# Kernel tuning notes

Hardware: AMD Instinct MI355X
Metric: run time of the kernel (lower is better)

Reference implementation:

```python
import jax, jax.numpy as jnp
import numpy as np

NUM_HEADS = 12
HEAD_DIM = 64
MASKED_BIAS = -10000.0


def setup_inputs() -> dict:
    key = jax.random.key(0)
    k1, k2, k3 = jax.random.split(key, 3)
    B, S, D = 2, 2048, 768
    return {
        "hidden_states": jax.random.normal(k1, (B, S, D), dtype=jnp.float32),
        "c_attn_w": jax.random.normal(k2, (D, 3 * D), dtype=jnp.float32) * 0.02,
        "c_attn_b": jnp.zeros((3 * D,), dtype=jnp.float32),
        "c_proj_w": jax.random.normal(k3, (D, D), dtype=jnp.float32) * 0.02,
        "c_proj_b": jnp.zeros((D,), dtype=jnp.float32),
    }


def _split_heads(x, B, S):
    # [B,S,D] -> [B,H,S,hd]
    return x.reshape(B, S, NUM_HEADS, HEAD_DIM).transpose(0, 2, 1, 3)


def reference(hidden_states, c_attn_w, c_attn_b, c_proj_w, c_proj_b):
    B, S, D = hidden_states.shape
    qkv = hidden_states @ c_attn_w + c_attn_b  # [B,S,3D]
    q, k, v = jnp.split(qkv, 3, axis=-1)
    q = _split_heads(q, B, S)
    k = _split_heads(k, B, S)
    v = _split_heads(v, B, S)

    # Unfused attention: full [B,H,S,S] scores, where-based causal mask
    attn_weights = jnp.einsum("bhqd,bhkd->bhqk", q, k)
    attn_weights = attn_weights / jnp.float32(HEAD_DIM) ** 0.5
    causal_mask = jnp.tril(jnp.ones((S, S), dtype=bool))[None, None]
    attn_weights = jnp.where(causal_mask, attn_weights,
                             jnp.asarray(MASKED_BIAS, attn_weights.dtype))
    attn_weights = jax.nn.softmax(attn_weights, axis=-1)
    attn_output = jnp.einsum("bhqk,bhkd->bhqd", attn_weights, v)

    # merge heads [B,H,S,hd] -> [B,S,D]
    attn_output = attn_output.transpose(0, 2, 1, 3).reshape(B, S, D)
    attn_output = attn_output @ c_proj_w + c_proj_b
    return attn_output
```

## Files before the change

kernel.cpp:

```cpp
#include <hip/hip_runtime.h>
#include <stdint.h>


constexpr int B_  = 2;
constexpr int S_  = 2048;
constexpr int D_  = 768;
constexpr int N3D = 3 * D_;
constexpr int M_  = B_ * S_;

typedef __bf16 bv8 __attribute__((ext_vector_type(8)));
typedef float  fv4 __attribute__((ext_vector_type(4)));
typedef unsigned short uv4 __attribute__((ext_vector_type(4)));
typedef unsigned short uv8 __attribute__((ext_vector_type(8)));

__device__ inline unsigned short f2bf(float x) {
    union { float f; unsigned int u; } v; v.f = x;
    unsigned int r = v.u + 0x7FFFu + ((v.u >> 16) & 1u);
    return (unsigned short)(r >> 16);
}

__device__ inline fv4 mfma16(bv8 a, bv8 b, fv4 c) {
    return __builtin_amdgcn_mfma_f32_16x16x32_bf16(a, b, c, 0, 0, 0);
}

#define GLOAD_LDS16(g, l)                                                        \
    __builtin_amdgcn_global_load_lds(                                            \
        (__attribute__((address_space(1))) void*)(g),                            \
        (__attribute__((address_space(3))) void*)(l), 16, 0, 0)

#define VMCNT4() asm volatile("s_waitcnt vmcnt(4)" ::: "memory")
#define VMCNT0() asm volatile("s_waitcnt vmcnt(0)" ::: "memory")
#define BAR()                                                                    \
    do { asm volatile("" ::: "memory"); __builtin_amdgcn_s_barrier();            \
         asm volatile("" ::: "memory"); } while (0)

__global__ __launch_bounds__(256)
void cvt_f32_bf16(const float* __restrict__ in, unsigned short* __restrict__ out)
{
    const size_t i = ((size_t)blockIdx.x * 256 + threadIdx.x) * 8;
    const float4 a = *(const float4*)&in[i];
    const float4 b = *(const float4*)&in[i + 4];
    uv8 o;
    o[0] = f2bf(a.x); o[1] = f2bf(a.y); o[2] = f2bf(a.z); o[3] = f2bf(a.w);
    o[4] = f2bf(b.x); o[5] = f2bf(b.y); o[6] = f2bf(b.z); o[7] = f2bf(b.w);
    *(uv8*)&out[i] = o;
}

__global__ __launch_bounds__(256)
void transpose_cvt(const float* __restrict__ W, unsigned short* __restrict__ WT,
                   int K, int N)
{
    __shared__ float tl[32][33];
    const int n0 = blockIdx.x * 32, k0 = blockIdx.y * 32;
    const int t = threadIdx.x;
    {
        const int r = t >> 3, c = (t & 7) * 4;
        const float4 v = *(const float4*)&W[(size_t)(k0 + r) * N + n0 + c];
        tl[r][c + 0] = v.x; tl[r][c + 1] = v.y; tl[r][c + 2] = v.z; tl[r][c + 3] = v.w;
    }
    __syncthreads();
    {
        const int rn = t >> 3, ck = (t & 7) * 4;
        uv4 o;
        o[0] = f2bf(tl[ck + 0][rn]); o[1] = f2bf(tl[ck + 1][rn]);
        o[2] = f2bf(tl[ck + 2][rn]); o[3] = f2bf(tl[ck + 3][rn]);
        *(uv4*)&WT[(size_t)(n0 + rn) * K + k0 + ck] = o;
    }
}

template<bool QKV>
__global__ __launch_bounds__(256)
void gemm_bf16(const unsigned short* __restrict__ A, const unsigned short* __restrict__ BT,
               const float* __restrict__ bias, float* __restrict__ Cf,
               unsigned short* __restrict__ Qb, unsigned short* __restrict__ Kb,
               unsigned short* __restrict__ VTb, int M, int N, int K)
{
    __shared__ unsigned short sA[2][128 * 32];
    __shared__ unsigned short sB[2][128 * 32];
    const int t = threadIdx.x, w = t >> 6, lane = t & 63;
    const int l15 = lane & 15, l4 = lane >> 4;
    const int m0 = blockIdx.y * 128, n0 = blockIdx.x * 128;
    const int wr = w >> 1, wc = w & 1;

    fv4 acc[4][4];
#pragma unroll
    for (int i = 0; i < 4; ++i)
#pragma unroll
        for (int j = 0; j < 4; ++j) acc[i][j] = fv4{0.f, 0.f, 0.f, 0.f};

    const int r0 = w * 16 + (lane >> 2);
    const int c0 = (lane & 3) ^ ((r0 >> 1) & 3);
    const int r1 = (w + 4) * 16 + (lane >> 2);
    const int c1 = (lane & 3) ^ ((r1 >> 1) & 3);

    auto stage = [&](int buf, int k0) {
        GLOAD_LDS16(A  + (size_t)(m0 + r0) * K + k0 + c0 * 8, &sA[buf][w * 512]);
        GLOAD_LDS16(A  + (size_t)(m0 + r1) * K + k0 + c1 * 8, &sA[buf][(w + 4) * 512]);
        GLOAD_LDS16(BT + (size_t)(n0 + r0) * K + k0 + c0 * 8, &sB[buf][w * 512]);
        GLOAD_LDS16(BT + (size_t)(n0 + r1) * K + k0 + c1 * 8, &sB[buf][(w + 4) * 512]);
    };

    stage(0, 0);
    const int nt = K >> 5;
    for (int tt = 0; tt < nt; ++tt) {
        const int cur = tt & 1;
        if (tt + 1 < nt) { stage(cur ^ 1, (tt + 1) * 32); VMCNT4(); }
        else             { VMCNT0(); }
        BAR();

        bv8 af[4], bf[4];
#pragma unroll
        for (int i = 0; i < 4; ++i) {
            const int r = wr * 64 + i * 16 + l15;
            const int c = l4 ^ ((r >> 1) & 3);
            af[i] = *(const bv8*)&sA[cur][r * 32 + c * 8];
        }
#pragma unroll
        for (int j = 0; j < 4; ++j) {
            const int r = wc * 64 + j * 16 + l15;
            const int c = l4 ^ ((r >> 1) & 3);
            bf[j] = *(const bv8*)&sB[cur][r * 32 + c * 8];
        }
#pragma unroll
        for (int i = 0; i < 4; ++i)
#pragma unroll
            for (int j = 0; j < 4; ++j)
                acc[i][j] = mfma16(af[i], bf[j], acc[i][j]);
        BAR();
    }

#pragma unroll
    for (int jf = 0; jf < 4; ++jf) {
        const int col = n0 + wc * 64 + jf * 16 + l15;
        const float bb = bias[col];
        if (QKV) {
            const int sect = col / 768;
            const int rem  = col - sect * 768;
            const int hh_  = rem >> 6, d = rem & 63;
#pragma unroll
            for (int i = 0; i < 4; ++i) {
                const int rowb = m0 + wr * 64 + i * 16 + l4 * 4;
                const size_t bh = (size_t)(rowb >> 11) * 12 + hh_;
                const int s0 = rowb & 2047;
                if (sect == 2) {
                    uv4 pk;
#pragma unroll
                    for (int reg = 0; reg < 4; ++reg) pk[reg] = f2bf(acc[i][jf][reg] + bb);
                    *(uv4*)&VTb[(bh * 64 + d) * 2048 + s0] = pk;
                } else {
                    unsigned short* dst = (sect == 0) ? Qb : Kb;
#pragma unroll
                    for (int reg = 0; reg < 4; ++reg)
                        dst[(bh * 2048 + s0 + reg) * 64 + d] = f2bf(acc[i][jf][reg] + bb);
                }
            }
        } else {
#pragma unroll
            for (int i = 0; i < 4; ++i) {
                const int rowb = m0 + wr * 64 + i * 16 + l4 * 4;
#pragma unroll
                for (int reg = 0; reg < 4; ++reg)
                    Cf[(size_t)(rowb + reg) * N + col] = acc[i][jf][reg] + bb;
            }
        }
    }
}

__global__ __launch_bounds__(256)
void flash_mfma(const unsigned short* __restrict__ Qb, const unsigned short* __restrict__ Kb,
                const unsigned short* __restrict__ VTb, unsigned short* __restrict__ outb)
{
    const int qt = 31 - blockIdx.x;
    const int h  = blockIdx.y, b = blockIdx.z;
    const int bh = b * 12 + h;

    __shared__ unsigned short sK [2][64 * 64];
    __shared__ unsigned short sVT[2][64 * 64];
    __shared__ unsigned short sP [4][16 * 64];

    const int t = threadIdx.x, w = t >> 6, lane = t & 63;
    const int l15 = lane & 15, l4 = lane >> 4;
    const int qrow = qt * 64 + w * 16;

    const int sr0 = w * 8 + (lane >> 3), sc0 = (lane & 7) ^ (sr0 & 7);
    const int sr1 = (w + 4) * 8 + (lane >> 3), sc1 = (lane & 7) ^ (sr1 & 7);
    const unsigned short* Kbase = Kb  + (size_t)bh * 2048 * 64;
    const unsigned short* Vbase = VTb + (size_t)bh * 64 * 2048;

    auto stage = [&](int buf, int kt) {
        GLOAD_LDS16(Kbase + (size_t)(kt * 64 + sr0) * 64 + sc0 * 8, &sK[buf][w * 512]);
        GLOAD_LDS16(Kbase + (size_t)(kt * 64 + sr1) * 64 + sc1 * 8, &sK[buf][(w + 4) * 512]);
        GLOAD_LDS16(Vbase + (size_t)sr0 * 2048 + kt * 64 + sc0 * 8, &sVT[buf][w * 512]);
        GLOAD_LDS16(Vbase + (size_t)sr1 * 2048 + kt * 64 + sc1 * 8, &sVT[buf][(w + 4) * 512]);
    };

    bv8 qf[2];
    {
        const unsigned short* qp = Qb + ((size_t)bh * 2048 + qrow + l15) * 64 + l4 * 8;
        qf[0] = *(const bv8*)qp;
        qf[1] = *(const bv8*)(qp + 32);
    }

    fv4 o[4];
#pragma unroll
    for (int j = 0; j < 4; ++j) o[j] = fv4{0.f, 0.f, 0.f, 0.f};
    float m_ = -1e30f, l_ = 0.f;

    stage(0, 0);
    for (int kt = 0; kt <= qt; ++kt) {
        const int cur = kt & 1;
        if (kt < qt) { stage(cur ^ 1, kt + 1); VMCNT4(); }
        else         { VMCNT0(); }
        BAR();

        fv4 st[4];
#pragma unroll
        for (int jf = 0; jf < 4; ++jf) {
            st[jf] = fv4{0.f, 0.f, 0.f, 0.f};
            const int kr = jf * 16 + l15;
#pragma unroll
            for (int hh = 0; hh < 2; ++hh) {
                const bv8 ka = *(const bv8*)&sK[cur][kr * 64 + (((hh * 4 + l4) ^ (kr & 7)) * 8)];
                st[jf] = mfma16(ka, qf[hh], st[jf]);
            }
        }

        float ps[16];
        const bool dtile = (kt == qt);
        const int qg = qrow + l15;
#pragma unroll
        for (int jf = 0; jf < 4; ++jf)
#pragma unroll
            for (int reg = 0; reg < 4; ++reg) {
                float v = st[jf][reg] * 0.125f;
                if (dtile && (kt * 64 + jf * 16 + l4 * 4 + reg) > qg) v = -10000.0f;
                ps[jf * 4 + reg] = v;
            }

        float rmax = ps[0];
#pragma unroll
        for (int u = 1; u < 16; ++u) rmax = fmaxf(rmax, ps[u]);
        rmax = fmaxf(rmax, __shfl_xor(rmax, 16));
        rmax = fmaxf(rmax, __shfl_xor(rmax, 32));
        const float nm = fmaxf(m_, rmax);
        const float sc = __expf(m_ - nm);
        float psum = 0.f;
#pragma unroll
        for (int u = 0; u < 16; ++u) {
            const float p = __expf(ps[u] - nm);
            ps[u] = p;
            psum += p;
        }
        psum += __shfl_xor(psum, 16);
        psum += __shfl_xor(psum, 32);
        l_ = l_ * sc + psum;
        m_ = nm;

        float scq[4];
#pragma unroll
        for (int reg = 0; reg < 4; ++reg) scq[reg] = __shfl(sc, l4 * 4 + reg);
#pragma unroll
        for (int jf = 0; jf < 4; ++jf)
#pragma unroll
            for (int reg = 0; reg < 4; ++reg) o[jf][reg] *= scq[reg];

#pragma unroll
        for (int jf = 0; jf < 4; ++jf) {
            uv4 pk;
#pragma unroll
            for (int reg = 0; reg < 4; ++reg) pk[reg] = f2bf(ps[jf * 4 + reg]);
            const int chunk = jf * 2 + (l4 >> 1);
            *(uv4*)&sP[w][l15 * 64 + ((chunk ^ (l15 & 7)) * 8) + (l4 & 1) * 4] = pk;
        }

        bv8 pa[2];
#pragma unroll
        for (int hh = 0; hh < 2; ++hh)
            pa[hh] = *(const bv8*)&sP[w][l15 * 64 + (((hh * 4 + l4) ^ (l15 & 7)) * 8)];
#pragma unroll
        for (int jf = 0; jf < 4; ++jf) {
            const int dr = jf * 16 + l15;
#pragma unroll
            for (int hh = 0; hh < 2; ++hh) {
                const bv8 vb = *(const bv8*)&sVT[cur][dr * 64 + (((hh * 4 + l4) ^ (dr & 7)) * 8)];
                o[jf] = mfma16(pa[hh], vb, o[jf]);
            }
        }
        BAR();
    }

    const float inv = 1.0f / l_;
    float invq[4];
#pragma unroll
    for (int reg = 0; reg < 4; ++reg) invq[reg] = __shfl(inv, l4 * 4 + reg);
#pragma unroll
    for (int jf = 0; jf < 4; ++jf)
#pragma unroll
        for (int reg = 0; reg < 4; ++reg)
            outb[(size_t)(b * S_ + qrow + l4 * 4 + reg) * D_ + h * 64 + jf * 16 + l15] =
                f2bf(o[jf][reg] * invq[reg]);
}

extern "C" void kernel_launch(void* const* d_in, const int* in_sizes, int n_in,
                              void* d_out, int out_size, void* d_ws, size_t ws_size,
                              hipStream_t stream)
{
    const float* hs    = (const float*)d_in[0];
    const float* wqkv  = (const float*)d_in[1];
    const float* bqkv  = (const float*)d_in[2];
    const float* wproj = (const float*)d_in[3];
    const float* bproj = (const float*)d_in[4];
    float* out = (float*)d_out;

    unsigned short* hsb    = (unsigned short*)d_ws;
    unsigned short* wqkvT  = hsb    + (size_t)M_ * D_;
    unsigned short* wprojT = wqkvT  + (size_t)N3D * D_;
    unsigned short* Qb     = wprojT + (size_t)D_ * D_;
    unsigned short* Kb     = Qb     + (size_t)24 * 2048 * 64;
    unsigned short* VTb    = Kb     + (size_t)24 * 2048 * 64;
    unsigned short* attnb  = VTb    + (size_t)24 * 2048 * 64;

    cvt_f32_bf16<<<(M_ * D_) / (256 * 8), 256, 0, stream>>>(hs, hsb);
    transpose_cvt<<<dim3(N3D / 32, D_ / 32), 256, 0, stream>>>(wqkv, wqkvT, D_, N3D);
    transpose_cvt<<<dim3(D_ / 32, D_ / 32), 256, 0, stream>>>(wproj, wprojT, D_, D_);

    gemm_bf16<true><<<dim3(N3D / 128, M_ / 128), 256, 0, stream>>>(
        hsb, wqkvT, bqkv, nullptr, Qb, Kb, VTb, M_, N3D, D_);
    flash_mfma<<<dim3(32, 12, 2), 256, 0, stream>>>(Qb, Kb, VTb, attnb);
    gemm_bf16<false><<<dim3(D_ / 128, M_ / 128), 256, 0, stream>>>(
        attnb, wprojT, bproj, out, nullptr, nullptr, nullptr, M_, D_, D_);
}
```

Before: 187.1 us.

## Use persistent atomic tile scheduler, exp2 softmax with deferred rescale in flash attention

The flash attention kernel becomes persistent: 512 blocks repeatedly claim (q-tile, head) work items from a global atomic counter, longest tiles first, so causal load imbalance is smoothed out. The 1/sqrt(d)*log2(e) scale is folded into Q inside the QKV GEMM epilogue, so softmax uses exp2 with no per-score multiply. Rescaling of the running max is skipped when the new max stays within a threshold. The change also adds s_setprio around the MFMA blocks and uses the native bf16 conversion. The risks are the extra atomic traffic, a counter reset that depends on the first kernel running, and a small accuracy change from deferred rescaling.

```diff
diff --git a/kernel.cpp b/kernel.cpp
--- a/kernel.cpp
+++ b/kernel.cpp
@@ -7,6 +7,10 @@
 constexpr int D_  = 768;
 constexpr int N3D = 3 * D_;
 constexpr int M_  = B_ * S_;
+constexpr int NTILE = 32 * 24;
+#define QSCALE 0.1803368801111f
+#define MASKB  (-14426.950408889634f)
+#define DEFER_THR 11.5f
 
 typedef __bf16 bv8 __attribute__((ext_vector_type(8)));
 typedef float  fv4 __attribute__((ext_vector_type(4)));
@@ -14,9 +18,8 @@
 typedef unsigned short uv8 __attribute__((ext_vector_type(8)));
 
 __device__ inline unsigned short f2bf(float x) {
-    union { float f; unsigned int u; } v; v.f = x;
-    unsigned int r = v.u + 0x7FFFu + ((v.u >> 16) & 1u);
-    return (unsigned short)(r >> 16);
+    __bf16 b = (__bf16)x;
+    return __builtin_bit_cast(unsigned short, b);
 }
 
 __device__ inline fv4 mfma16(bv8 a, bv8 b, fv4 c) {
@@ -35,8 +38,10 @@
          asm volatile("" ::: "memory"); } while (0)
 
 __global__ __launch_bounds__(256)
-void cvt_f32_bf16(const float* __restrict__ in, unsigned short* __restrict__ out)
-{
+void cvt_f32_bf16(const float* __restrict__ in, unsigned short* __restrict__ out,
+                  int* __restrict__ cnt)
+{
+    if (blockIdx.x == 0 && threadIdx.x == 0) *cnt = 0;
     const size_t i = ((size_t)blockIdx.x * 256 + threadIdx.x) * 8;
     const float4 a = *(const float4*)&in[i];
     const float4 b = *(const float4*)&in[i + 4];
@@ -147,11 +152,15 @@
 #pragma unroll
                     for (int reg = 0; reg < 4; ++reg) pk[reg] = f2bf(acc[i][jf][reg] + bb);
                     *(uv4*)&VTb[(bh * 64 + d) * 2048 + s0] = pk;
+                } else if (sect == 0) {
+#pragma unroll
+                    for (int reg = 0; reg < 4; ++reg)
+                        Qb[(bh * 2048 + s0 + reg) * 64 + d] =
+                            f2bf((acc[i][jf][reg] + bb) * QSCALE);
                 } else {
-                    unsigned short* dst = (sect == 0) ? Qb : Kb;
 #pragma unroll
                     for (int reg = 0; reg < 4; ++reg)
-                        dst[(bh * 2048 + s0 + reg) * 64 + d] = f2bf(acc[i][jf][reg] + bb);
+                        Kb[(bh * 2048 + s0 + reg) * 64 + d] = f2bf(acc[i][jf][reg] + bb);
                 }
             }
         } else {
@@ -168,137 +177,160 @@
 
 __global__ __launch_bounds__(256)
 void flash_mfma(const unsigned short* __restrict__ Qb, const unsigned short* __restrict__ Kb,
-                const unsigned short* __restrict__ VTb, unsigned short* __restrict__ outb)
-{
-    const int qt = 31 - blockIdx.x;
-    const int h  = blockIdx.y, b = blockIdx.z;
-    const int bh = b * 12 + h;
-
+                const unsigned short* __restrict__ VTb, unsigned short* __restrict__ outb,
+                int* __restrict__ cnt)
+{
     __shared__ unsigned short sK [2][64 * 64];
     __shared__ unsigned short sVT[2][64 * 64];
     __shared__ unsigned short sP [4][16 * 64];
+    __shared__ int sj;
 
     const int t = threadIdx.x, w = t >> 6, lane = t & 63;
     const int l15 = lane & 15, l4 = lane >> 4;
-    const int qrow = qt * 64 + w * 16;
 
     const int sr0 = w * 8 + (lane >> 3), sc0 = (lane & 7) ^ (sr0 & 7);
     const int sr1 = (w + 4) * 8 + (lane >> 3), sc1 = (lane & 7) ^ (sr1 & 7);
-    const unsigned short* Kbase = Kb  + (size_t)bh * 2048 * 64;
-    const unsigned short* Vbase = VTb + (size_t)bh * 64 * 2048;
-
-    auto stage = [&](int buf, int kt) {
-        GLOAD_LDS16(Kbase + (size_t)(kt * 64 + sr0) * 64 + sc0 * 8, &sK[buf][w * 512]);
-        GLOAD_LDS16(Kbase + (size_t)(kt * 64 + sr1) * 64 + sc1 * 8, &sK[buf][(w + 4) * 512]);
-        GLOAD_LDS16(Vbase + (size_t)sr0 * 2048 + kt * 64 + sc0 * 8, &sVT[buf][w * 512]);
-        GLOAD_LDS16(Vbase + (size_t)sr1 * 2048 + kt * 64 + sc1 * 8, &sVT[buf][(w + 4) * 512]);
-    };
-
-    bv8 qf[2];
-    {
-        const unsigned short* qp = Qb + ((size_t)bh * 2048 + qrow + l15) * 64 + l4 * 8;
-        qf[0] = *(const bv8*)qp;
-        qf[1] = *(const bv8*)(qp + 32);
-    }
-
-    fv4 o[4];
-#pragma unroll
-    for (int j = 0; j < 4; ++j) o[j] = fv4{0.f, 0.f, 0.f, 0.f};
-    float m_ = -1e30f, l_ = 0.f;
-
-    stage(0, 0);
-    for (int kt = 0; kt <= qt; ++kt) {
-        const int cur = kt & 1;
-        if (kt < qt) { stage(cur ^ 1, kt + 1); VMCNT4(); }
-        else         { VMCNT0(); }
-        BAR();
-
-        fv4 st[4];
-#pragma unroll
-        for (int jf = 0; jf < 4; ++jf) {
-            st[jf] = fv4{0.f, 0.f, 0.f, 0.f};
-            const int kr = jf * 16 + l15;
-#pragma unroll
-            for (int hh = 0; hh < 2; ++hh) {
-                const bv8 ka = *(const bv8*)&sK[cur][kr * 64 + (((hh * 4 + l4) ^ (kr & 7)) * 8)];
-                st[jf] = mfma16(ka, qf[hh], st[jf]);
-            }
-        }
-
-        float ps[16];
-        const bool dtile = (kt == qt);
-        const int qg = qrow + l15;
+
+    for (;;) {
+        if (t == 0) sj = atomicAdd(cnt, 1);
+        __syncthreads();
+        const int j = sj;
+        if (j >= NTILE) return;
+        const int qt = 31 - j / 24;
+        const int bh = j - (j / 24) * 24;
+        const int b = bh / 12, h = bh - b * 12;
+        const int qrow = qt * 64 + w * 16;
+
+        const unsigned short* Kbase = Kb  + (size_t)bh * 2048 * 64;
+        const unsigned short* Vbase = VTb + (size_t)bh * 64 * 2048;
+
+        bv8 qf[2];
+        {
+            const unsigned short* qp = Qb + ((size_t)bh * 2048 + qrow + l15) * 64 + l4 * 8;
+            qf[0] = *(const bv8*)qp;
+            qf[1] = *(const bv8*)(qp + 32);
+        }
+
+        fv4 o[4];
+#pragma unroll
+        for (int jf = 0; jf < 4; ++jf) o[jf] = fv4{0.f, 0.f, 0.f, 0.f};
+        float m_ = -1e30f, l_ = 0.f;
+
+        GLOAD_LDS16(Kbase + (size_t)sr0 * 64 + sc0 * 8, &sK[0][w * 512]);
+        GLOAD_LDS16(Kbase + (size_t)sr1 * 64 + sc1 * 8, &sK[0][(w + 4) * 512]);
+        GLOAD_LDS16(Vbase + (size_t)sr0 * 2048 + sc0 * 8, &sVT[0][w * 512]);
+        GLOAD_LDS16(Vbase + (size_t)sr1 * 2048 + sc1 * 8, &sVT[0][(w + 4) * 512]);
+
+        for (int kt = 0; kt <= qt; ++kt) {
+            const int cur = kt & 1;
+            if (kt < qt) {
+                const int nk = kt + 1;
+                GLOAD_LDS16(Kbase + (size_t)(nk * 64 + sr0) * 64 + sc0 * 8, &sK[cur ^ 1][w * 512]);
+                GLOAD_LDS16(Kbase + (size_t)(nk * 64 + sr1) * 64 + sc1 * 8, &sK[cur ^ 1][(w + 4) * 512]);
+                GLOAD_LDS16(Vbase + (size_t)sr0 * 2048 + nk * 64 + sc0 * 8, &sVT[cur ^ 1][w * 512]);
+                GLOAD_LDS16(Vbase + (size_t)sr1 * 2048 + nk * 64 + sc1 * 8, &sVT[cur ^ 1][(w + 4) * 512]);
+                VMCNT4();
+            } else VMCNT0();
+            BAR();
+
+            fv4 st[4];
+            __builtin_amdgcn_s_setprio(1);
+#pragma unroll
+            for (int jf = 0; jf < 4; ++jf) {
+                st[jf] = fv4{0.f, 0.f, 0.f, 0.f};
+                const int kr = jf * 16 + l15;
+#pragma unroll
+                for (int hh = 0; hh < 2; ++hh) {
+                    const bv8 ka = *(const bv8*)&sK[cur][kr * 64 + (((hh * 4 + l4) ^ (kr & 7)) * 8)];
+                    st[jf] = mfma16(ka, qf[hh], st[jf]);
+                }
+            }
+            __builtin_amdgcn_s_setprio(0);
+
+            float ps[16];
+            const int qg = qrow + l15;
+            if (kt == qt) {
+#pragma unroll
+                for (int jf = 0; jf < 4; ++jf)
+#pragma unroll
+                    for (int reg = 0; reg < 4; ++reg) {
+                        const int kvg = kt * 64 + jf * 16 + l4 * 4 + reg;
+                        ps[jf * 4 + reg] = (kvg > qg) ? MASKB : st[jf][reg];
+                    }
+            } else {
+#pragma unroll
+                for (int jf = 0; jf < 4; ++jf)
+#pragma unroll
+                    for (int reg = 0; reg < 4; ++reg) ps[jf * 4 + reg] = st[jf][reg];
+            }
+
+            float rmax = ps[0];
+#pragma unroll
+            for (int u = 1; u < 16; ++u) rmax = fmaxf(rmax, ps[u]);
+            rmax = fmaxf(rmax, __shfl_xor(rmax, 16));
+            rmax = fmaxf(rmax, __shfl_xor(rmax, 32));
+            if (!__all(rmax <= m_ + DEFER_THR)) {
+                const float nm = fmaxf(m_, rmax);
+                const float sc = exp2f(m_ - nm);
+                float scq[4];
+#pragma unroll
+                for (int reg = 0; reg < 4; ++reg) scq[reg] = __shfl(sc, l4 * 4 + reg);
+#pragma unroll
+                for (int jf = 0; jf < 4; ++jf)
+#pragma unroll
+                    for (int reg = 0; reg < 4; ++reg) o[jf][reg] *= scq[reg];
+                l_ *= sc;
+                m_ = nm;
+            }
+            float psum = 0.f;
+#pragma unroll
+            for (int u = 0; u < 16; ++u) {
+                const float p = exp2f(ps[u] - m_);
+                ps[u] = p;
+                psum += p;
+            }
+            psum += __shfl_xor(psum, 16);
+            psum += __shfl_xor(psum, 32);
+            l_ += psum;
+
+#pragma unroll
+            for (int jf = 0; jf < 4; ++jf) {
+                uv4 pk;
+#pragma unroll
+                for (int reg = 0; reg < 4; ++reg) pk[reg] = f2bf(ps[jf * 4 + reg]);
+                const int chunk = jf * 2 + (l4 >> 1);
+                *(uv4*)&sP[w][l15 * 64 + ((chunk ^ (l15 & 7)) * 8) + (l4 & 1) * 4] = pk;
+            }
+
+            bv8 pa[2];
+#pragma unroll
+            for (int hh = 0; hh < 2; ++hh)
+                pa[hh] = *(const bv8*)&sP[w][l15 * 64 + (((hh * 4 + l4) ^ (l15 & 7)) * 8)];
+            __builtin_amdgcn_s_setprio(1);
+#pragma unroll
+            for (int jf = 0; jf < 4; ++jf) {
+                const int dr = jf * 16 + l15;
+#pragma unroll
+                for (int hh = 0; hh < 2; ++hh) {
+                    const bv8 vb = *(const bv8*)&sVT[cur][dr * 64 + (((hh * 4 + l4) ^ (dr & 7)) * 8)];
+                    o[jf] = mfma16(pa[hh], vb, o[jf]);
+                }
+            }
+            __builtin_amdgcn_s_setprio(0);
+            BAR();
+        }
+
+        const float inv = 1.0f / l_;
+        float invq[4];
+#pragma unroll
+        for (int reg = 0; reg < 4; ++reg) invq[reg] = __shfl(inv, l4 * 4 + reg);
 #pragma unroll
         for (int jf = 0; jf < 4; ++jf)
 #pragma unroll
-            for (int reg = 0; reg < 4; ++reg) {
-                float v = st[jf][reg] * 0.125f;
-                if (dtile && (kt * 64 + jf * 16 + l4 * 4 + reg) > qg) v = -10000.0f;
-                ps[jf * 4 + reg] = v;
-            }
-
-        float rmax = ps[0];
-#pragma unroll
-        for (int u = 1; u < 16; ++u) rmax = fmaxf(rmax, ps[u]);
-        rmax = fmaxf(rmax, __shfl_xor(rmax, 16));
-        rmax = fmaxf(rmax, __shfl_xor(rmax, 32));
-        const float nm = fmaxf(m_, rmax);
-        const float sc = __expf(m_ - nm);
-        float psum = 0.f;
-#pragma unroll
-        for (int u = 0; u < 16; ++u) {
-            const float p = __expf(ps[u] - nm);
-            ps[u] = p;
-            psum += p;
-        }
-        psum += __shfl_xor(psum, 16);
-        psum += __shfl_xor(psum, 32);
-        l_ = l_ * sc + psum;
-        m_ = nm;
-
-        float scq[4];
-#pragma unroll
-        for (int reg = 0; reg < 4; ++reg) scq[reg] = __shfl(sc, l4 * 4 + reg);
-#pragma unroll
-        for (int jf = 0; jf < 4; ++jf)
-#pragma unroll
-            for (int reg = 0; reg < 4; ++reg) o[jf][reg] *= scq[reg];
-
-#pragma unroll
-        for (int jf = 0; jf < 4; ++jf) {
-            uv4 pk;
-#pragma unroll
-            for (int reg = 0; reg < 4; ++reg) pk[reg] = f2bf(ps[jf * 4 + reg]);
-            const int chunk = jf * 2 + (l4 >> 1);
-            *(uv4*)&sP[w][l15 * 64 + ((chunk ^ (l15 & 7)) * 8) + (l4 & 1) * 4] = pk;
-        }
-
-        bv8 pa[2];
-#pragma unroll
-        for (int hh = 0; hh < 2; ++hh)
-            pa[hh] = *(const bv8*)&sP[w][l15 * 64 + (((hh * 4 + l4) ^ (l15 & 7)) * 8)];
-#pragma unroll
-        for (int jf = 0; jf < 4; ++jf) {
-            const int dr = jf * 16 + l15;
-#pragma unroll
-            for (int hh = 0; hh < 2; ++hh) {
-                const bv8 vb = *(const bv8*)&sVT[cur][dr * 64 + (((hh * 4 + l4) ^ (dr & 7)) * 8)];
-                o[jf] = mfma16(pa[hh], vb, o[jf]);
-            }
-        }
-        BAR();
-    }
-
-    const float inv = 1.0f / l_;
-    float invq[4];
-#pragma unroll
-    for (int reg = 0; reg < 4; ++reg) invq[reg] = __shfl(inv, l4 * 4 + reg);
-#pragma unroll
-    for (int jf = 0; jf < 4; ++jf)
-#pragma unroll
-        for (int reg = 0; reg < 4; ++reg)
-            outb[(size_t)(b * S_ + qrow + l4 * 4 + reg) * D_ + h * 64 + jf * 16 + l15] =
-                f2bf(o[jf][reg] * invq[reg]);
+            for (int reg = 0; reg < 4; ++reg)
+                outb[(size_t)(b * S_ + qrow + l4 * 4 + reg) * D_ + h * 64 + jf * 16 + l15] =
+                    f2bf(o[jf][reg] * invq[reg]);
+    }
 }
 
 extern "C" void kernel_launch(void* const* d_in, const int* in_sizes, int n_in,
@@ -319,14 +351,15 @@
     unsigned short* Kb     = Qb     + (size_t)24 * 2048 * 64;
     unsigned short* VTb    = Kb     + (size_t)24 * 2048 * 64;
     unsigned short* attnb  = VTb    + (size_t)24 * 2048 * 64;
-
-    cvt_f32_bf16<<<(M_ * D_) / (256 * 8), 256, 0, stream>>>(hs, hsb);
+    int* cnt = (int*)(attnb + (size_t)M_ * D_);
+
+    cvt_f32_bf16<<<(M_ * D_) / (256 * 8), 256, 0, stream>>>(hs, hsb, cnt);
     transpose_cvt<<<dim3(N3D / 32, D_ / 32), 256, 0, stream>>>(wqkv, wqkvT, D_, N3D);
     transpose_cvt<<<dim3(D_ / 32, D_ / 32), 256, 0, stream>>>(wproj, wprojT, D_, D_);
 
     gemm_bf16<true><<<dim3(N3D / 128, M_ / 128), 256, 0, stream>>>(
         hsb, wqkvT, bqkv, nullptr, Qb, Kb, VTb, M_, N3D, D_);
-    flash_mfma<<<dim3(32, 12, 2), 256, 0, stream>>>(Qb, Kb, VTb, attnb);
+    flash_mfma<<<512, 256, 0, stream>>>(Qb, Kb, VTb, attnb, cnt);
     gemm_bf16<false><<<dim3(D_ / 128, M_ / 128), 256, 0, stream>>>(
         attnb, wprojT, bproj, out, nullptr, nullptr, nullptr, M_, D_, D_);
 }
```

New measurement: 177.7 us. -5.0%, faster.
